# Performance work log

Hardware: AMD Instinct MI355X
Metric: run time of the kernel (lower is better)

The kernel has to match this reference:

```python
import jax, jax.numpy as jnp
import numpy as np

B, N, C_IN, C_OUT = 4, 8192, 16, 16
N_LAYERS = 3
OUT = 2

def setup_inputs() -> dict:
    key = jax.random.key(0)
    k1, k2, k3, k4, k5, k6 = jax.random.split(key, 6)
    node_features = jax.random.normal(k1, (B, N, C_IN), dtype=jnp.float32)
    # dense weighted adjacency in [0,1); rows sum to ~N/2 so degree-normalize is well-defined
    adj_matrix = jax.random.uniform(k2, (B, N, N), dtype=jnp.float32)
    s_proj = 1.0 / np.sqrt(C_IN)
    W_proj = jax.random.uniform(k3, (C_OUT, C_IN), jnp.float32, -s_proj, s_proj)
    b_proj = jax.random.uniform(k4, (C_OUT,), jnp.float32, -s_proj, s_proj)
    s_fl = 1.0 / np.sqrt(N * C_OUT)
    W_fl = jax.random.uniform(k5, (OUT, N * C_OUT), jnp.float32, -s_fl, s_fl)
    b_fl = jax.random.uniform(k6, (OUT,), jnp.float32, -s_fl, s_fl)
    return {"node_features": node_features, "adj_matrix": adj_matrix,
            "W_proj": W_proj, "b_proj": b_proj, "W_fl": W_fl, "b_fl": b_fl}

def reference(node_features, adj_matrix, W_proj, b_proj, W_fl, b_fl):
    # degree (row-sum) is constant across layers; compute once  [B, N, 1]
    deg = jnp.sum(adj_matrix, axis=-1, keepdims=True)
    h = node_features
    for _ in range(N_LAYERS):
        h = h @ W_proj.T + b_proj                        # shared Linear projection [B,N,C]
        h = jnp.einsum('bij,bjc->bic', adj_matrix, h)    # adjacency bmm aggregation
        h = jax.nn.relu(h / deg)                         # degree-normalize + ReLU
    h = h.reshape(h.shape[0], -1)                        # [B, N*C]
    h = jnp.where(jnp.isnan(h), 0.0, h)                  # vectorized NaN scrub
    return h @ W_fl.T + b_fl                             # [B, 2]
```

## Files before the change

kernel.cpp:

```cpp
#include <hip/hip_runtime.h>

#define B_ 4
#define N_ 8192
#define C_ 16
#define JT 512
#define NT (N_ / JT)
#define LSTR (JT + 8)

#define JTC 256
#define NTC (N_ / JTC)
#define CLB (JTC + 8)
#define HSH (JTC + 4)

typedef _Float16 f16;
typedef f16   f16x2 __attribute__((ext_vector_type(2)));
typedef f16   f16x4 __attribute__((ext_vector_type(4)));
typedef f16   f16x8 __attribute__((ext_vector_type(8)));
typedef float fv4   __attribute__((ext_vector_type(4)));
typedef float f32x4 __attribute__((ext_vector_type(4)));
typedef unsigned int ui2 __attribute__((ext_vector_type(2)));

union v8u { f16x8 v8; f16x2 v2[4]; unsigned int u[4]; };
union cvu { fv4 v; ui2 h[2]; };

__device__ __forceinline__ float fdot2(f16x2 a, f16x2 b, float c) {
    float d;
    asm("v_dot2_f32_f16 %0, %1, %2, %3" : "=v"(d) : "v"(a), "v"(b), "v"(c));
    return d;
}

#define DOT8(accv, au, hu)                          \
    do {                                            \
        accv = fdot2((au).v2[0], (hu).v2[0], accv); \
        accv = fdot2((au).v2[1], (hu).v2[1], accv); \
        accv = fdot2((au).v2[2], (hu).v2[2], accv); \
        accv = fdot2((au).v2[3], (hu).v2[3], accv); \
    } while (0)

__device__ __forceinline__ unsigned int enc1(float f) {
    f16 h = (f16)f;
    unsigned short us = __builtin_bit_cast(unsigned short, h);
    return ((unsigned int)us + 32u) >> 6;
}
__device__ __forceinline__ void dec4(unsigned int d, f16x2& p01, f16x2& p23) {
#if __has_builtin(__builtin_amdgcn_perm)
    unsigned int t0 = __builtin_amdgcn_perm(d, d, 0x0C010C00u) << 6;
    unsigned int t1 = __builtin_amdgcn_perm(d, d, 0x0C030C02u) << 6;
#else
    unsigned int t0 = ((d & 0xFFu) | ((d << 8) & 0x00FF0000u)) << 6;
    unsigned int t1 = (((d >> 16) & 0xFFu) | ((d >> 8) & 0x00FF0000u)) << 6;
#endif
    p01 = __builtin_bit_cast(f16x2, t0);
    p23 = __builtin_bit_cast(f16x2, t1);
}
__device__ __forceinline__ void dec8(ui2 d, v8u& out) {
    dec4(d.x, out.v2[0], out.v2[1]);
    dec4(d.y, out.v2[2], out.v2[3]);
}

__global__ __launch_bounds__(256) void proj_t_kernel(const float* __restrict__ hin,
                                                     const float* __restrict__ W,
                                                     const float* __restrict__ bias,
                                                     f16* __restrict__ hT) {
    __shared__ float Ws[C_ * C_];
    __shared__ float bs[C_];
    int t = threadIdx.x;
    Ws[t] = W[t];
    if (t < C_) bs[t] = bias[t];
    __syncthreads();
    int nn = blockIdx.x * 256 + t;
    int b = nn >> 13, n = nn & (N_ - 1);
    const fv4* hv = (const fv4*)(hin + (size_t)nn * C_);
    fv4 q0 = hv[0], q1 = hv[1], q2 = hv[2], q3 = hv[3];
    float hr[16] = {q0[0], q0[1], q0[2], q0[3], q1[0], q1[1], q1[2], q1[3],
                    q2[0], q2[1], q2[2], q2[3], q3[0], q3[1], q3[2], q3[3]};
    f16* dst = hT + ((size_t)b * C_) * N_ + n;
#pragma unroll
    for (int c = 0; c < 16; ++c) {
        float s = bs[c];
#pragma unroll
        for (int k = 0; k < 16; ++k) s += hr[k] * Ws[c * 16 + k];
        dst[(size_t)c * N_] = (f16)s;
    }
}

__global__ __launch_bounds__(256) void agg0_kernel(const float* __restrict__ adjf,
                                                   unsigned char* __restrict__ adjc_out,
                                                   const f16* __restrict__ hTin,
                                                   float* __restrict__ deg,
                                                   const float* __restrict__ Wp,
                                                   const float* __restrict__ bp,
                                                   f16* __restrict__ hTout) {
    __shared__ f16 hs[2][C_][LSTR];
    __shared__ float Ws[C_ * C_ + C_];
    __shared__ float accL[4][4][C_ + 1];

    const int b = blockIdx.y;
    const int i0 = blockIdx.x * 16;
    const int t = threadIdx.x;
    const int wave = t >> 6, lane = t & 63;
    const int r0 = i0 + wave * 4;

    Ws[t] = Wp[t];
    if (t < C_) Ws[C_ * C_ + t] = bp[t];

    const f16* hTb = hTin + (size_t)b * C_ * N_;
    const int srow = t >> 4, schunk = t & 15;
    auto stage = [&](int buf, int jt) {
        const f16* src = hTb + (size_t)srow * N_ + jt + schunk * 8;
#pragma unroll
        for (int k = 0; k < 4; ++k) {
            f16x8 v = *(const f16x8*)(src + k * 128);
            *(f16x8*)&hs[buf][srow][schunk * 8 + k * 128] = v;
        }
    };

    size_t arow[4];
#pragma unroll
    for (int r = 0; r < 4; ++r) arow[r] = ((size_t)b * N_ + (r0 + r)) * (size_t)N_;

    float acc[4][C_];
#pragma unroll
    for (int r = 0; r < 4; ++r)
#pragma unroll
        for (int c = 0; c < C_; ++c) acc[r][c] = 0.f;
    float ds4[4] = {0.f, 0.f, 0.f, 0.f};
    const f16x2 ones = {(f16)1.f, (f16)1.f};

    fv4 pf0[4], pf1[4];
    auto load_adj = [&](int jb) {
#pragma unroll
        for (int r = 0; r < 4; ++r) {
            pf0[r] = __builtin_nontemporal_load((const fv4*)(adjf + arow[r] + jb));
            pf1[r] = __builtin_nontemporal_load((const fv4*)(adjf + arow[r] + jb) + 1);
        }
    };

    load_adj(lane * 8);
    stage(0, 0);

    for (int tile = 0; tile < NT; ++tile) {
        __syncthreads();
        if (tile + 1 < NT) stage((tile + 1) & 1, (tile + 1) * JT);
        const int buf = tile & 1;
        const int jb = tile * JT + lane * 8;

        fv4 c0[4], c1[4];
#pragma unroll
        for (int r = 0; r < 4; ++r) { c0[r] = pf0[r]; c1[r] = pf1[r]; }
        if (tile + 1 < NT) load_adj((tile + 1) * JT + lane * 8);

        v8u av[4];
#pragma unroll
        for (int r = 0; r < 4; ++r) {
            ui2 pk;
            pk.x = enc1(c0[r][0]) | (enc1(c0[r][1]) << 8) |
                   (enc1(c0[r][2]) << 16) | (enc1(c0[r][3]) << 24);
            pk.y = enc1(c1[r][0]) | (enc1(c1[r][1]) << 8) |
                   (enc1(c1[r][2]) << 16) | (enc1(c1[r][3]) << 24);
            *(ui2*)(adjc_out + arow[r] + jb) = pk;
            dec8(pk, av[r]);
        }
        v8u on; on.v2[0] = ones; on.v2[1] = ones; on.v2[2] = ones; on.v2[3] = ones;
#pragma unroll
        for (int r = 0; r < 4; ++r) DOT8(ds4[r], av[r], on);

#pragma unroll
        for (int c = 0; c < C_; ++c) {
            v8u hu;
            hu.v8 = *(const f16x8*)&hs[buf][c][lane * 8];
            DOT8(acc[0][c], av[0], hu);
            DOT8(acc[1][c], av[1], hu);
            DOT8(acc[2][c], av[2], hu);
            DOT8(acc[3][c], av[3], hu);
        }
    }

    float dv[4];
#pragma unroll
    for (int r = 0; r < 4; ++r)
#pragma unroll
        for (int c = 0; c < C_; ++c) {
            float v = acc[r][c];
#pragma unroll
            for (int m = 32; m >= 1; m >>= 1) v += __shfl_xor(v, m, 64);
            acc[r][c] = v;
        }
#pragma unroll
    for (int r = 0; r < 4; ++r) {
        float v = ds4[r];
#pragma unroll
        for (int m = 32; m >= 1; m >>= 1) v += __shfl_xor(v, m, 64);
        dv[r] = v;
    }
    if (lane == 0) {
#pragma unroll
        for (int r = 0; r < 4; ++r) deg[(size_t)b * N_ + r0 + r] = dv[r];
#pragma unroll
        for (int r = 0; r < 4; ++r)
#pragma unroll
            for (int c = 0; c < C_; ++c) accL[wave][r][c] = acc[r][c];
    }
    __syncthreads();

    if (lane < C_) {
        const int ec = lane;
#pragma unroll
        for (int r = 0; r < 4; ++r) {
            float p = Ws[C_ * C_ + ec];
#pragma unroll
            for (int c = 0; c < C_; ++c) {
                float o = accL[wave][r][c] / dv[r];
                o = o > 0.f ? o : 0.f;
                p += o * Ws[ec * C_ + c];
            }
            hTout[(size_t)b * C_ * N_ + (size_t)ec * N_ + (r0 + r)] = (f16)p;
        }
    }
}

template <int MODE>
__global__ __launch_bounds__(256) void aggm_kernel(const unsigned char* __restrict__ adjc,
                                                   const f16* __restrict__ hTin,
                                                   const float* __restrict__ deg,
                                                   const float* __restrict__ Wp,
                                                   const float* __restrict__ bp,
                                                   f16* __restrict__ hTout,
                                                   float* __restrict__ gout) {
    __shared__ unsigned char cl[2][64][CLB];
    __shared__ f16 hs[2][C_][HSH];
    __shared__ float accL[4][16][C_ + 1];
    __shared__ float Ws[C_ * C_ + C_];

    const int b = blockIdx.y;
    const int i0 = blockIdx.x * 64;
    const int t = threadIdx.x;
    const int wave = t >> 6, lane = t & 63;
    const int m = lane & 15, kg = lane >> 4;

    if (MODE == 1) {
        Ws[t] = Wp[t];
        if (t < C_) Ws[C_ * C_ + t] = bp[t];
    }

    const int crow = t >> 2, coff = (t & 3) * 64;
    const int hrow = t >> 4, hoff = (t & 15) * 16;
    const unsigned char* cbase = adjc + ((size_t)b * N_ + i0 + crow) * (size_t)N_;
    const f16* hbase = hTin + (size_t)b * C_ * N_ + (size_t)hrow * N_;

    fv4 creg[4];
    f16x8 hreg0, hreg1;
    auto ld_regs = [&](int jt) {
#pragma unroll
        for (int k = 0; k < 4; ++k)
            creg[k] = *(const fv4*)(cbase + jt + coff + k * 16);
        hreg0 = *(const f16x8*)(hbase + jt + hoff);
        hreg1 = *(const f16x8*)(hbase + jt + hoff + 8);
    };
    auto st_lds = [&](int buf) {
#pragma unroll
        for (int k = 0; k < 4; ++k) {
            cvu cc; cc.v = creg[k];
            *(ui2*)&cl[buf][crow][coff + k * 16] = cc.h[0];
            *(ui2*)&cl[buf][crow][coff + k * 16 + 8] = cc.h[1];
        }
        union { f16x8 v; f16x4 q[2]; } h0, h1;
        h0.v = hreg0; h1.v = hreg1;
        *(f16x4*)&hs[buf][hrow][hoff + 0]  = h0.q[0];
        *(f16x4*)&hs[buf][hrow][hoff + 4]  = h0.q[1];
        *(f16x4*)&hs[buf][hrow][hoff + 8]  = h1.q[0];
        *(f16x4*)&hs[buf][hrow][hoff + 12] = h1.q[1];
    };

    f32x4 acc = {0.f, 0.f, 0.f, 0.f};
    const int arow_l = wave * 16 + m;

    ld_regs(0);
    for (int tile = 0; tile < NTC; ++tile) {
        const int buf = tile & 1;
        st_lds(buf);
        if (tile + 1 < NTC) ld_regs((tile + 1) * JTC);
        __syncthreads();
#pragma unroll
        for (int ks = 0; ks < JTC / 32; ++ks) {
            const int col = ks * 32 + kg * 8;
            ui2 cw = *(const ui2*)&cl[buf][arow_l][col];
            v8u a;
            dec4(cw.x, a.v2[0], a.v2[1]);
            dec4(cw.y, a.v2[2], a.v2[3]);
            v8u bf;
            ui2 b0 = *(const ui2*)&hs[buf][m][col];
            ui2 b1 = *(const ui2*)&hs[buf][m][col + 4];
            bf.u[0] = b0.x; bf.u[1] = b0.y; bf.u[2] = b1.x; bf.u[3] = b1.y;
            acc = __builtin_amdgcn_mfma_f32_16x16x32_f16(a.v8, bf.v8, acc, 0, 0, 0);
        }
    }

#pragma unroll
    for (int r = 0; r < 4; ++r)
        accL[wave][kg * 4 + r][m] = acc[r];
    __syncthreads();

#pragma unroll
    for (int it = 0; it < 4; ++it) {
        const int idx = t + it * 256;
        const int row = idx >> 4, ec = idx & 15;
        const int w2 = row >> 4, rl = row & 15;
        const float dvv = deg[(size_t)b * N_ + i0 + row];
        if (MODE == 1) {
            float p = Ws[C_ * C_ + ec];
#pragma unroll
            for (int c = 0; c < C_; ++c) {
                float o = accL[w2][rl][c] / dvv;
                o = o > 0.f ? o : 0.f;
                p += o * Ws[ec * C_ + c];
            }
            hTout[(size_t)b * C_ * N_ + (size_t)ec * N_ + (i0 + row)] = (f16)p;
        } else {
            float o = accL[w2][rl][ec] / dvv;
            gout[((size_t)b * N_ + i0 + row) * C_ + ec] = o > 0.f ? o : 0.f;
        }
    }
}

__global__ __launch_bounds__(256) void final_partial(const float* __restrict__ g,
                                                     const float* __restrict__ Wfl,
                                                     float* __restrict__ partial) {
    const int bx = blockIdx.x;
    const int b = bx >> 5, o = (bx >> 4) & 1, chunk = bx & 15;
    const size_t base = (size_t)chunk * 8192;
    const fv4* hv = (const fv4*)(g + (size_t)b * N_ * C_ + base);
    const fv4* wv = (const fv4*)(Wfl + (size_t)o * N_ * C_ + base);
    float s = 0.f;
#pragma unroll
    for (int k = 0; k < 8; ++k) {
        int idx = threadIdx.x + k * 256;
        fv4 a = hv[idx], w = wv[idx];
        s += a[0] * w[0] + a[1] * w[1] + a[2] * w[2] + a[3] * w[3];
    }
#pragma unroll
    for (int m = 32; m >= 1; m >>= 1) s += __shfl_xor(s, m, 64);
    __shared__ float wsum[4];
    if ((threadIdx.x & 63) == 0) wsum[threadIdx.x >> 6] = s;
    __syncthreads();
    if (threadIdx.x == 0) partial[bx] = wsum[0] + wsum[1] + wsum[2] + wsum[3];
}

__global__ void final_reduce(const float* __restrict__ partial,
                             const float* __restrict__ bfl,
                             float* __restrict__ out) {
    int i = threadIdx.x;
    if (i < B_ * 2) {
        float s = bfl[i & 1];
        for (int k = 0; k < 16; ++k) s += partial[i * 16 + k];
        out[i] = s;
    }
}

__global__ __launch_bounds__(256) void proj_kernel(const float* __restrict__ hin,
                                                   const float* __restrict__ W,
                                                   const float* __restrict__ bias,
                                                   float* __restrict__ hout,
                                                   int total_nodes) {
    __shared__ float Ws[C_ * C_];
    __shared__ float bs[C_];
    int t = threadIdx.x;
    if (t < C_ * C_) Ws[t] = W[t];
    if (t < C_) bs[t] = bias[t];
    __syncthreads();
    int n = blockIdx.x * 256 + t;
    if (n >= total_nodes) return;
    const fv4* hv = (const fv4*)(hin + (size_t)n * C_);
    fv4 q0 = hv[0], q1 = hv[1], q2 = hv[2], q3 = hv[3];
    float hr[16] = {q0[0], q0[1], q0[2], q0[3], q1[0], q1[1], q1[2], q1[3],
                    q2[0], q2[1], q2[2], q2[3], q3[0], q3[1], q3[2], q3[3]};
    float o[16];
#pragma unroll
    for (int c = 0; c < 16; ++c) {
        float s = bs[c];
#pragma unroll
        for (int k = 0; k < 16; ++k) s += hr[k] * Ws[c * 16 + k];
        o[c] = s;
    }
    fv4* ov = (fv4*)(hout + (size_t)n * C_);
    ov[0] = fv4{o[0], o[1], o[2], o[3]};
    ov[1] = fv4{o[4], o[5], o[6], o[7]};
    ov[2] = fv4{o[8], o[9], o[10], o[11]};
    ov[3] = fv4{o[12], o[13], o[14], o[15]};
}

__global__ __launch_bounds__(256) void agg_kernel_f32(const float* __restrict__ adj,
                                                      const float* __restrict__ hin,
                                                      float* __restrict__ hout) {
    __shared__ fv4 hsf[JT][5];
    const int b = blockIdx.y;
    const int i0 = blockIdx.x * 16;
    const int t = threadIdx.x;
    const int wave = t >> 6;
    const int lane = t & 63;
    const int r0 = i0 + wave * 4;
    const float* adjb = adj + (size_t)b * N_ * N_;
    const float* hb = hin + (size_t)b * N_ * C_;
    const float* ar[4];
#pragma unroll
    for (int r = 0; r < 4; ++r) ar[r] = adjb + (size_t)(r0 + r) * N_;
    float acc[4][16];
#pragma unroll
    for (int r = 0; r < 4; ++r)
#pragma unroll
        for (int c = 0; c < 16; ++c) acc[r][c] = 0.f;
    float rs[4] = {0.f, 0.f, 0.f, 0.f};
    for (int jt = 0; jt < N_; jt += JT) {
        const fv4* src = (const fv4*)(hb + (size_t)jt * C_);
#pragma unroll
        for (int k = 0; k < (JT * C_ / 4) / 256; ++k) {
            int g = t + k * 256;
            hsf[g >> 2][g & 3] = src[g];
        }
        __syncthreads();
#pragma unroll 2
        for (int jj = lane; jj < JT; jj += 64) {
            fv4 q0 = hsf[jj][0], q1 = hsf[jj][1], q2 = hsf[jj][2], q3 = hsf[jj][3];
            float hv[16] = {q0[0], q0[1], q0[2], q0[3], q1[0], q1[1], q1[2], q1[3],
                            q2[0], q2[1], q2[2], q2[3], q3[0], q3[1], q3[2], q3[3]};
#pragma unroll
            for (int r = 0; r < 4; ++r) {
                float av = ar[r][jt + jj];
                rs[r] += av;
#pragma unroll
                for (int c = 0; c < 16; ++c) acc[r][c] += av * hv[c];
            }
        }
        __syncthreads();
    }
#pragma unroll
    for (int r = 0; r < 4; ++r) {
#pragma unroll
        for (int c = 0; c < 16; ++c) {
            float v = acc[r][c];
            for (int mm = 32; mm >= 1; mm >>= 1) v += __shfl_xor(v, mm, 64);
            acc[r][c] = v;
        }
        float d = rs[r];
        for (int mm = 32; mm >= 1; mm >>= 1) d += __shfl_xor(d, mm, 64);
        rs[r] = d;
    }
    if (lane == 0) {
#pragma unroll
        for (int r = 0; r < 4; ++r) {
            float inv = 1.0f / rs[r];
            fv4* dst = (fv4*)(hout + (size_t)b * N_ * C_ + (size_t)(r0 + r) * C_);
#pragma unroll
            for (int q = 0; q < 4; ++q) {
                fv4 ov;
#pragma unroll
                for (int e = 0; e < 4; ++e) {
                    float v = acc[r][q * 4 + e] * inv;
                    ov[e] = v > 0.f ? v : 0.f;
                }
                dst[q] = ov;
            }
        }
    }
}

extern "C" void kernel_launch(void* const* d_in, const int* in_sizes, int n_in,
                              void* d_out, int out_size, void* d_ws, size_t ws_size,
                              hipStream_t stream) {
    const float* x   = (const float*)d_in[0];
    const float* adj = (const float*)d_in[1];
    const float* Wp  = (const float*)d_in[2];
    const float* bp  = (const float*)d_in[3];
    const float* Wfl = (const float*)d_in[4];
    const float* bfl = (const float*)d_in[5];
    float* out = (float*)d_out;

    const size_t adjc_b = (size_t)B_ * N_ * N_;
    const size_t deg_b  = (size_t)B_ * N_ * sizeof(float);
    const size_t hT_b   = (size_t)B_ * C_ * N_ * sizeof(f16);
    const size_t g_b    = (size_t)B_ * N_ * C_ * sizeof(float);
    const size_t part_b = 128 * sizeof(float);

    if (ws_size >= adjc_b + deg_b + 2 * hT_b + g_b + part_b) {
        char* p = (char*)d_ws;
        unsigned char* adjc = (unsigned char*)p; p += adjc_b;
        float* deg     = (float*)p; p += deg_b;
        f16* hTa       = (f16*)p;   p += hT_b;
        f16* hTb       = (f16*)p;   p += hT_b;
        float* g       = (float*)p; p += g_b;
        float* partial = (float*)p;

        const int pblocks = B_ * N_ / 256;
        dim3 ag0(N_ / 16, B_);
        dim3 agm(N_ / 64, B_);

        proj_t_kernel<<<pblocks, 256, 0, stream>>>(x, Wp, bp, hTa);
        agg0_kernel<<<ag0, 256, 0, stream>>>(adj, adjc, hTa, deg, Wp, bp, hTb);
        aggm_kernel<1><<<agm, 256, 0, stream>>>(adjc, hTb, deg, Wp, bp, hTa, nullptr);
        aggm_kernel<2><<<agm, 256, 0, stream>>>(adjc, hTa, deg, Wp, bp, nullptr, g);
        final_partial<<<B_ * 32, 256, 0, stream>>>(g, Wfl, partial);
        final_reduce<<<1, 64, 0, stream>>>(partial, bfl, out);
    } else {
        float* hA = (float*)d_ws;
        float* hB = hA + (size_t)B_ * N_ * C_;
        float* partial = hB + (size_t)B_ * N_ * C_;
        const int nodes = B_ * N_;
        dim3 aggGrid(N_ / 16, B_);
        proj_kernel<<<(nodes + 255) / 256, 256, 0, stream>>>(x, Wp, bp, hA, nodes);
        agg_kernel_f32<<<aggGrid, 256, 0, stream>>>(adj, hA, hB);
        proj_kernel<<<(nodes + 255) / 256, 256, 0, stream>>>(hB, Wp, bp, hA, nodes);
        agg_kernel_f32<<<aggGrid, 256, 0, stream>>>(adj, hA, hB);
        proj_kernel<<<(nodes + 255) / 256, 256, 0, stream>>>(hB, Wp, bp, hA, nodes);
        agg_kernel_f32<<<aggGrid, 256, 0, stream>>>(adj, hA, hB);
        final_partial<<<B_ * 32, 256, 0, stream>>>(hB, Wfl, partial);
        final_reduce<<<1, 64, 0, stream>>>(partial, bfl, out);
    }
}
```

Before: 393.7 us.

## Rewrite first aggregation layer with MFMA tiles and LDS-staged compressed adjacency

Replaces the dot2-based first aggregation kernel, which gave each wave 4 rows and reduced across lanes with shuffles, with a 64-row-per-block kernel. It stages the encoded 8-bit adjacency and the f16 features through LDS and accumulates with 16x16x32 f16 MFMA, as the later layers already do. Each thread still reads fp32 adjacency, encodes it, writes the compressed copy and accumulates the degree. The aim is to cut ALU and shuffle-reduction work so the pass that streams the 1 GB fp32 adjacency stays bandwidth-bound, at the cost of more LDS traffic and a barrier per 128-column tile.

```diff
diff --git a/kernel.cpp b/kernel.cpp
--- a/kernel.cpp
+++ b/kernel.cpp
@@ -3,14 +3,20 @@
 #define B_ 4
 #define N_ 8192
 #define C_ 16
-#define JT 512
-#define NT (N_ / JT)
-#define LSTR (JT + 8)
+
+#define JT0 128
+#define NT0 (N_ / JT0)
+#define CLB0 (JT0 + 8)
+#define HSH0 (JT0 + 4)
 
 #define JTC 256
 #define NTC (N_ / JTC)
 #define CLB (JTC + 8)
 #define HSH (JTC + 4)
+
+#define JT 512
+#define NT (N_ / JT)
+#define LSTR (JT + 8)
 
 typedef _Float16 f16;
 typedef f16   f16x2 __attribute__((ext_vector_type(2)));
@@ -19,23 +25,15 @@
 typedef float fv4   __attribute__((ext_vector_type(4)));
 typedef float f32x4 __attribute__((ext_vector_type(4)));
 typedef unsigned int ui2 __attribute__((ext_vector_type(2)));
+typedef unsigned int ui4 __attribute__((ext_vector_type(4)));
 
 union v8u { f16x8 v8; f16x2 v2[4]; unsigned int u[4]; };
-union cvu { fv4 v; ui2 h[2]; };
 
 __device__ __forceinline__ float fdot2(f16x2 a, f16x2 b, float c) {
     float d;
     asm("v_dot2_f32_f16 %0, %1, %2, %3" : "=v"(d) : "v"(a), "v"(b), "v"(c));
     return d;
 }
-
-#define DOT8(accv, au, hu)                          \
-    do {                                            \
-        accv = fdot2((au).v2[0], (hu).v2[0], accv); \
-        accv = fdot2((au).v2[1], (hu).v2[1], accv); \
-        accv = fdot2((au).v2[2], (hu).v2[2], accv); \
-        accv = fdot2((au).v2[3], (hu).v2[3], accv); \
-    } while (0)
 
 __device__ __forceinline__ unsigned int enc1(float f) {
     f16 h = (f16)f;
@@ -53,10 +51,6 @@
     p01 = __builtin_bit_cast(f16x2, t0);
     p23 = __builtin_bit_cast(f16x2, t1);
 }
-__device__ __forceinline__ void dec8(ui2 d, v8u& out) {
-    dec4(d.x, out.v2[0], out.v2[1]);
-    dec4(d.y, out.v2[2], out.v2[3]);
-}
 
 __global__ __launch_bounds__(256) void proj_t_kernel(const float* __restrict__ hin,
                                                      const float* __restrict__ W,
@@ -84,138 +78,123 @@
     }
 }
 
-__global__ __launch_bounds__(256) void agg0_kernel(const float* __restrict__ adjf,
-                                                   unsigned char* __restrict__ adjc_out,
-                                                   const f16* __restrict__ hTin,
-                                                   float* __restrict__ deg,
-                                                   const float* __restrict__ Wp,
-                                                   const float* __restrict__ bp,
-                                                   f16* __restrict__ hTout) {
-    __shared__ f16 hs[2][C_][LSTR];
+__global__ __launch_bounds__(256) void agg0m_kernel(const float* __restrict__ adjf,
+                                                    unsigned char* __restrict__ adjc_out,
+                                                    const f16* __restrict__ hTin,
+                                                    float* __restrict__ deg,
+                                                    const float* __restrict__ Wp,
+                                                    const float* __restrict__ bp,
+                                                    f16* __restrict__ hTout) {
+    __shared__ unsigned char cl[2][64][CLB0];
+    __shared__ f16 hs[2][C_][HSH0];
+    __shared__ float accL[4][16][C_ + 1];
     __shared__ float Ws[C_ * C_ + C_];
-    __shared__ float accL[4][4][C_ + 1];
+    __shared__ float dpart[64][5];
+    __shared__ float degf[64];
 
     const int b = blockIdx.y;
-    const int i0 = blockIdx.x * 16;
+    const int i0 = blockIdx.x * 64;
     const int t = threadIdx.x;
     const int wave = t >> 6, lane = t & 63;
-    const int r0 = i0 + wave * 4;
+    const int m = lane & 15, kg = lane >> 4;
 
     Ws[t] = Wp[t];
     if (t < C_) Ws[C_ * C_ + t] = bp[t];
 
-    const f16* hTb = hTin + (size_t)b * C_ * N_;
-    const int srow = t >> 4, schunk = t & 15;
-    auto stage = [&](int buf, int jt) {
-        const f16* src = hTb + (size_t)srow * N_ + jt + schunk * 8;
+    const int crow = t >> 2, cq = t & 3, coff = cq * 32;
+    const int hrow = t >> 4, hoff = (t & 15) * 8;
+    const float* abase = adjf + ((size_t)b * N_ + i0 + crow) * (size_t)N_;
+    unsigned char* cobase = adjc_out + ((size_t)b * N_ + i0 + crow) * (size_t)N_;
+    const f16* hbase = hTin + (size_t)b * C_ * N_ + (size_t)hrow * N_;
+
+    fv4 areg[8];
+    f16x8 hreg;
+    auto ld_regs = [&](int jt) {
+#pragma unroll
+        for (int k = 0; k < 8; ++k)
+            areg[k] = __builtin_nontemporal_load((const fv4*)(abase + jt + coff + k * 4));
+        hreg = *(const f16x8*)(hbase + jt + hoff);
+    };
+
+    f32x4 acc = {0.f, 0.f, 0.f, 0.f};
+    float dsum = 0.f;
+    const f16x2 ones = {(f16)1.f, (f16)1.f};
+    const int arow_l = wave * 16 + m;
+
+    ld_regs(0);
+    for (int tile = 0; tile < NT0; ++tile) {
+        const int buf = tile & 1;
+        unsigned int cw[8];
+#pragma unroll
+        for (int k = 0; k < 8; ++k) {
+            cw[k] = enc1(areg[k][0]) | (enc1(areg[k][1]) << 8) |
+                    (enc1(areg[k][2]) << 16) | (enc1(areg[k][3]) << 24);
+        }
 #pragma unroll
         for (int k = 0; k < 4; ++k) {
-            f16x8 v = *(const f16x8*)(src + k * 128);
-            *(f16x8*)&hs[buf][srow][schunk * 8 + k * 128] = v;
-        }
-    };
-
-    size_t arow[4];
-#pragma unroll
-    for (int r = 0; r < 4; ++r) arow[r] = ((size_t)b * N_ + (r0 + r)) * (size_t)N_;
-
-    float acc[4][C_];
-#pragma unroll
-    for (int r = 0; r < 4; ++r)
-#pragma unroll
-        for (int c = 0; c < C_; ++c) acc[r][c] = 0.f;
-    float ds4[4] = {0.f, 0.f, 0.f, 0.f};
-    const f16x2 ones = {(f16)1.f, (f16)1.f};
-
-    fv4 pf0[4], pf1[4];
-    auto load_adj = [&](int jb) {
-#pragma unroll
-        for (int r = 0; r < 4; ++r) {
-            pf0[r] = __builtin_nontemporal_load((const fv4*)(adjf + arow[r] + jb));
-            pf1[r] = __builtin_nontemporal_load((const fv4*)(adjf + arow[r] + jb) + 1);
-        }
-    };
-
-    load_adj(lane * 8);
-    stage(0, 0);
-
-    for (int tile = 0; tile < NT; ++tile) {
+            ui2 w; w.x = cw[2 * k]; w.y = cw[2 * k + 1];
+            *(ui2*)&cl[buf][crow][coff + k * 8] = w;
+        }
+        {
+            ui4 s0 = {cw[0], cw[1], cw[2], cw[3]};
+            ui4 s1 = {cw[4], cw[5], cw[6], cw[7]};
+            *(ui4*)(cobase + tile * JT0 + coff) = s0;
+            *(ui4*)(cobase + tile * JT0 + coff + 16) = s1;
+        }
+        {
+            union { f16x8 v; f16x4 q[2]; } hh; hh.v = hreg;
+            *(f16x4*)&hs[buf][hrow][hoff] = hh.q[0];
+            *(f16x4*)&hs[buf][hrow][hoff + 4] = hh.q[1];
+        }
+#pragma unroll
+        for (int k = 0; k < 8; ++k) {
+            f16x2 p01, p23;
+            dec4(cw[k], p01, p23);
+            dsum = fdot2(p01, ones, dsum);
+            dsum = fdot2(p23, ones, dsum);
+        }
+        if (tile + 1 < NT0) ld_regs((tile + 1) * JT0);
         __syncthreads();
-        if (tile + 1 < NT) stage((tile + 1) & 1, (tile + 1) * JT);
-        const int buf = tile & 1;
-        const int jb = tile * JT + lane * 8;
-
-        fv4 c0[4], c1[4];
-#pragma unroll
-        for (int r = 0; r < 4; ++r) { c0[r] = pf0[r]; c1[r] = pf1[r]; }
-        if (tile + 1 < NT) load_adj((tile + 1) * JT + lane * 8);
-
-        v8u av[4];
-#pragma unroll
-        for (int r = 0; r < 4; ++r) {
-            ui2 pk;
-            pk.x = enc1(c0[r][0]) | (enc1(c0[r][1]) << 8) |
-                   (enc1(c0[r][2]) << 16) | (enc1(c0[r][3]) << 24);
-            pk.y = enc1(c1[r][0]) | (enc1(c1[r][1]) << 8) |
-                   (enc1(c1[r][2]) << 16) | (enc1(c1[r][3]) << 24);
-            *(ui2*)(adjc_out + arow[r] + jb) = pk;
-            dec8(pk, av[r]);
-        }
-        v8u on; on.v2[0] = ones; on.v2[1] = ones; on.v2[2] = ones; on.v2[3] = ones;
-#pragma unroll
-        for (int r = 0; r < 4; ++r) DOT8(ds4[r], av[r], on);
-
+#pragma unroll
+        for (int ks = 0; ks < JT0 / 32; ++ks) {
+            const int col = ks * 32 + kg * 8;
+            ui2 cwv = *(const ui2*)&cl[buf][arow_l][col];
+            v8u a;
+            dec4(cwv.x, a.v2[0], a.v2[1]);
+            dec4(cwv.y, a.v2[2], a.v2[3]);
+            v8u bf;
+            ui2 b0 = *(const ui2*)&hs[buf][m][col];
+            ui2 b1 = *(const ui2*)&hs[buf][m][col + 4];
+            bf.u[0] = b0.x; bf.u[1] = b0.y; bf.u[2] = b1.x; bf.u[3] = b1.y;
+            acc = __builtin_amdgcn_mfma_f32_16x16x32_f16(a.v8, bf.v8, acc, 0, 0, 0);
+        }
+    }
+
+    dpart[crow][cq] = dsum;
+#pragma unroll
+    for (int r = 0; r < 4; ++r) accL[wave][kg * 4 + r][m] = acc[r];
+    __syncthreads();
+    if (t < 64) {
+        float d = dpart[t][0] + dpart[t][1] + dpart[t][2] + dpart[t][3];
+        degf[t] = d;
+        deg[(size_t)b * N_ + i0 + t] = d;
+    }
+    __syncthreads();
+
+#pragma unroll
+    for (int it = 0; it < 4; ++it) {
+        const int idx = t + it * 256;
+        const int row = idx >> 4, ec = idx & 15;
+        const int w2 = row >> 4, rl = row & 15;
+        const float dvv = degf[row];
+        float p = Ws[C_ * C_ + ec];
 #pragma unroll
         for (int c = 0; c < C_; ++c) {
-            v8u hu;
-            hu.v8 = *(const f16x8*)&hs[buf][c][lane * 8];
-            DOT8(acc[0][c], av[0], hu);
-            DOT8(acc[1][c], av[1], hu);
-            DOT8(acc[2][c], av[2], hu);
-            DOT8(acc[3][c], av[3], hu);
-        }
-    }
-
-    float dv[4];
-#pragma unroll
-    for (int r = 0; r < 4; ++r)
-#pragma unroll
-        for (int c = 0; c < C_; ++c) {
-            float v = acc[r][c];
-#pragma unroll
-            for (int m = 32; m >= 1; m >>= 1) v += __shfl_xor(v, m, 64);
-            acc[r][c] = v;
-        }
-#pragma unroll
-    for (int r = 0; r < 4; ++r) {
-        float v = ds4[r];
-#pragma unroll
-        for (int m = 32; m >= 1; m >>= 1) v += __shfl_xor(v, m, 64);
-        dv[r] = v;
-    }
-    if (lane == 0) {
-#pragma unroll
-        for (int r = 0; r < 4; ++r) deg[(size_t)b * N_ + r0 + r] = dv[r];
-#pragma unroll
-        for (int r = 0; r < 4; ++r)
-#pragma unroll
-            for (int c = 0; c < C_; ++c) accL[wave][r][c] = acc[r][c];
-    }
-    __syncthreads();
-
-    if (lane < C_) {
-        const int ec = lane;
-#pragma unroll
-        for (int r = 0; r < 4; ++r) {
-            float p = Ws[C_ * C_ + ec];
-#pragma unroll
-            for (int c = 0; c < C_; ++c) {
-                float o = accL[wave][r][c] / dv[r];
-                o = o > 0.f ? o : 0.f;
-                p += o * Ws[ec * C_ + c];
-            }
-            hTout[(size_t)b * C_ * N_ + (size_t)ec * N_ + (r0 + r)] = (f16)p;
-        }
+            float o = accL[w2][rl][c] / dvv;
+            o = o > 0.f ? o : 0.f;
+            p += o * Ws[ec * C_ + c];
+        }
+        hTout[(size_t)b * C_ * N_ + (size_t)ec * N_ + (i0 + row)] = (f16)p;
     }
 }
 
@@ -260,7 +239,7 @@
     auto st_lds = [&](int buf) {
 #pragma unroll
         for (int k = 0; k < 4; ++k) {
-            cvu cc; cc.v = creg[k];
+            union { fv4 v; ui2 h[2]; } cc; cc.v = creg[k];
             *(ui2*)&cl[buf][crow][coff + k * 16] = cc.h[0];
             *(ui2*)&cl[buf][crow][coff + k * 16 + 8] = cc.h[1];
         }
@@ -491,11 +470,10 @@
         float* partial = (float*)p;
 
         const int pblocks = B_ * N_ / 256;
-        dim3 ag0(N_ / 16, B_);
         dim3 agm(N_ / 64, B_);
 
         proj_t_kernel<<<pblocks, 256, 0, stream>>>(x, Wp, bp, hTa);
-        agg0_kernel<<<ag0, 256, 0, stream>>>(adj, adjc, hTa, deg, Wp, bp, hTb);
+        agg0m_kernel<<<agm, 256, 0, stream>>>(adj, adjc, hTa, deg, Wp, bp, hTb);
         aggm_kernel<1><<<agm, 256, 0, stream>>>(adjc, hTb, deg, Wp, bp, hTa, nullptr);
         aggm_kernel<2><<<agm, 256, 0, stream>>>(adjc, hTa, deg, Wp, bp, nullptr, g);
         final_partial<<<B_ * 32, 256, 0, stream>>>(g, Wfl, partial);
```

Measured after the change: 640.1 us. 62.6% more time.

## Split first-layer aggregation into encode-only pass plus compressed aggm layer

Applied to the files above, without the earlier changes.

Breaks the fused first-layer kernel apart. A lean enc_kernel now only reads the fp32 adjacency, writes the 8-bit compressed copy and computes the degrees. The first layer's aggregation then runs through the existing aggm_kernel on the compressed adjacency. This drops the per-tile LDS staging, barriers and dot products from the fp32-bandwidth-bound pass. The cost is an extra full read of the 256 MB byte-compressed adjacency and one more launch.

```diff
diff --git a/kernel.cpp b/kernel.cpp
--- a/kernel.cpp
+++ b/kernel.cpp
@@ -5,12 +5,13 @@
 #define C_ 16
 #define JT 512
 #define NT (N_ / JT)
-#define LSTR (JT + 8)
 
 #define JTC 256
 #define NTC (N_ / JTC)
 #define CLB (JTC + 8)
 #define HSH (JTC + 4)
+
+#define LSTR (JT + 8)
 
 typedef _Float16 f16;
 typedef f16   f16x2 __attribute__((ext_vector_type(2)));
@@ -84,46 +85,19 @@
     }
 }
 
-__global__ __launch_bounds__(256) void agg0_kernel(const float* __restrict__ adjf,
-                                                   unsigned char* __restrict__ adjc_out,
-                                                   const f16* __restrict__ hTin,
-                                                   float* __restrict__ deg,
-                                                   const float* __restrict__ Wp,
-                                                   const float* __restrict__ bp,
-                                                   f16* __restrict__ hTout) {
-    __shared__ f16 hs[2][C_][LSTR];
-    __shared__ float Ws[C_ * C_ + C_];
-    __shared__ float accL[4][4][C_ + 1];
-
+__global__ __launch_bounds__(256) void enc_kernel(const float* __restrict__ adjf,
+                                                  unsigned char* __restrict__ adjc_out,
+                                                  float* __restrict__ deg) {
     const int b = blockIdx.y;
     const int i0 = blockIdx.x * 16;
     const int t = threadIdx.x;
     const int wave = t >> 6, lane = t & 63;
     const int r0 = i0 + wave * 4;
 
-    Ws[t] = Wp[t];
-    if (t < C_) Ws[C_ * C_ + t] = bp[t];
-
-    const f16* hTb = hTin + (size_t)b * C_ * N_;
-    const int srow = t >> 4, schunk = t & 15;
-    auto stage = [&](int buf, int jt) {
-        const f16* src = hTb + (size_t)srow * N_ + jt + schunk * 8;
-#pragma unroll
-        for (int k = 0; k < 4; ++k) {
-            f16x8 v = *(const f16x8*)(src + k * 128);
-            *(f16x8*)&hs[buf][srow][schunk * 8 + k * 128] = v;
-        }
-    };
-
     size_t arow[4];
 #pragma unroll
     for (int r = 0; r < 4; ++r) arow[r] = ((size_t)b * N_ + (r0 + r)) * (size_t)N_;
 
-    float acc[4][C_];
-#pragma unroll
-    for (int r = 0; r < 4; ++r)
-#pragma unroll
-        for (int c = 0; c < C_; ++c) acc[r][c] = 0.f;
     float ds4[4] = {0.f, 0.f, 0.f, 0.f};
     const f16x2 ones = {(f16)1.f, (f16)1.f};
 
@@ -137,20 +111,13 @@
     };
 
     load_adj(lane * 8);
-    stage(0, 0);
-
     for (int tile = 0; tile < NT; ++tile) {
-        __syncthreads();
-        if (tile + 1 < NT) stage((tile + 1) & 1, (tile + 1) * JT);
-        const int buf = tile & 1;
         const int jb = tile * JT + lane * 8;
-
         fv4 c0[4], c1[4];
 #pragma unroll
         for (int r = 0; r < 4; ++r) { c0[r] = pf0[r]; c1[r] = pf1[r]; }
         if (tile + 1 < NT) load_adj((tile + 1) * JT + lane * 8);
 
-        v8u av[4];
 #pragma unroll
         for (int r = 0; r < 4; ++r) {
             ui2 pk;
@@ -159,63 +126,18 @@
             pk.y = enc1(c1[r][0]) | (enc1(c1[r][1]) << 8) |
                    (enc1(c1[r][2]) << 16) | (enc1(c1[r][3]) << 24);
             *(ui2*)(adjc_out + arow[r] + jb) = pk;
-            dec8(pk, av[r]);
-        }
-        v8u on; on.v2[0] = ones; on.v2[1] = ones; on.v2[2] = ones; on.v2[3] = ones;
-#pragma unroll
-        for (int r = 0; r < 4; ++r) DOT8(ds4[r], av[r], on);
-
-#pragma unroll
-        for (int c = 0; c < C_; ++c) {
-            v8u hu;
-            hu.v8 = *(const f16x8*)&hs[buf][c][lane * 8];
-            DOT8(acc[0][c], av[0], hu);
-            DOT8(acc[1][c], av[1], hu);
-            DOT8(acc[2][c], av[2], hu);
-            DOT8(acc[3][c], av[3], hu);
-        }
-    }
-
-    float dv[4];
-#pragma unroll
-    for (int r = 0; r < 4; ++r)
-#pragma unroll
-        for (int c = 0; c < C_; ++c) {
-            float v = acc[r][c];
-#pragma unroll
-            for (int m = 32; m >= 1; m >>= 1) v += __shfl_xor(v, m, 64);
-            acc[r][c] = v;
-        }
+            v8u av; dec8(pk, av);
+            v8u on; on.v2[0] = ones; on.v2[1] = ones; on.v2[2] = ones; on.v2[3] = ones;
+            DOT8(ds4[r], av, on);
+        }
+    }
+
 #pragma unroll
     for (int r = 0; r < 4; ++r) {
         float v = ds4[r];
 #pragma unroll
         for (int m = 32; m >= 1; m >>= 1) v += __shfl_xor(v, m, 64);
-        dv[r] = v;
-    }
-    if (lane == 0) {
-#pragma unroll
-        for (int r = 0; r < 4; ++r) deg[(size_t)b * N_ + r0 + r] = dv[r];
-#pragma unroll
-        for (int r = 0; r < 4; ++r)
-#pragma unroll
-            for (int c = 0; c < C_; ++c) accL[wave][r][c] = acc[r][c];
-    }
-    __syncthreads();
-
-    if (lane < C_) {
-        const int ec = lane;
-#pragma unroll
-        for (int r = 0; r < 4; ++r) {
-            float p = Ws[C_ * C_ + ec];
-#pragma unroll
-            for (int c = 0; c < C_; ++c) {
-                float o = accL[wave][r][c] / dv[r];
-                o = o > 0.f ? o : 0.f;
-                p += o * Ws[ec * C_ + c];
-            }
-            hTout[(size_t)b * C_ * N_ + (size_t)ec * N_ + (r0 + r)] = (f16)p;
-        }
+        if (lane == 0) deg[(size_t)b * N_ + r0 + r] = v;
     }
 }
 
@@ -491,11 +413,12 @@
         float* partial = (float*)p;
 
         const int pblocks = B_ * N_ / 256;
-        dim3 ag0(N_ / 16, B_);
+        dim3 age(N_ / 16, B_);
         dim3 agm(N_ / 64, B_);
 
         proj_t_kernel<<<pblocks, 256, 0, stream>>>(x, Wp, bp, hTa);
-        agg0_kernel<<<ag0, 256, 0, stream>>>(adj, adjc, hTa, deg, Wp, bp, hTb);
+        enc_kernel<<<age, 256, 0, stream>>>(adj, adjc, deg);
+        aggm_kernel<1><<<agm, 256, 0, stream>>>(adjc, hTa, deg, Wp, bp, hTb, nullptr);
         aggm_kernel<1><<<agm, 256, 0, stream>>>(adjc, hTb, deg, Wp, bp, hTa, nullptr);
         aggm_kernel<2><<<agm, 256, 0, stream>>>(adjc, hTa, deg, Wp, bp, nullptr, g);
         final_partial<<<B_ * 32, 256, 0, stream>>>(g, Wfl, partial);
```

Result: slower. 410.7 us (+4.3%).
